# Kernel optimization log

Measured on AMD Instinct MI355X. Metric: run time of the kernel, lower is better.

Reference implementation:

```python
import jax, jax.numpy as jnp
import numpy as np

N = 50000        # nodes
E = 800000       # edges (avg degree 16)
NODE_D = 128     # node_attr_dim
EDGE_D = 16      # edge_attr_dim
HID = 300        # hidden_dim (module default)


def setup_inputs() -> dict:
    key = jax.random.key(0)
    ks = jax.random.split(key, 8)
    x = jax.random.normal(ks[0], (N, NODE_D), jnp.float32)
    edge_attr = jax.random.normal(ks[1], (E, EDGE_D), jnp.float32)
    edge_weight = jax.random.uniform(ks[2], (E,), jnp.float32)
    node_weight = jax.random.uniform(ks[3], (N,), jnp.float32)
    edge_index = jax.random.randint(ks[4], (2, E), 0, N, jnp.int32)
    # lin0: Linear(node_attr_dim + edge_attr_dim, hidden_dim)
    W0 = jax.random.normal(ks[5], (NODE_D + EDGE_D, HID), jnp.float32) / np.sqrt(NODE_D + EDGE_D)
    b0 = jnp.zeros((HID,), jnp.float32)
    # mp_layer.linear: Linear(hidden_dim, hidden_dim)
    W = jax.random.normal(ks[6], (HID, HID), jnp.float32) / np.sqrt(HID)
    b = jnp.zeros((HID,), jnp.float32)
    return dict(x=x, edge_attr=edge_attr, edge_weight=edge_weight,
                node_weight=node_weight, W0=W0, b0=b0, W=W, b=b,
                edge_index=edge_index)


def reference(x, edge_attr, edge_weight, node_weight, W0, b0, W, b, edge_index):
    src = edge_index[0]   # x_j (source, flow='source_to_target')
    dst = edge_index[1]   # aggregation target i
    n = x.shape[0]

    # --- isFirstLayer: weighted sum of incoming edge features, scattered at dst ---
    inc = jax.ops.segment_sum(edge_weight[:, None] * edge_attr, dst, num_segments=n)  # [N, EDGE_D]
    h0 = jax.nn.relu(jnp.concatenate([x, inc], axis=1) @ W0 + b0)                     # [N, HID]

    # --- MessagePassingLayer: message = edge_weight * x_j; aggr = mean at dst ---
    msg = edge_weight[:, None] * h0[src]                                              # [E, HID]
    agg = jax.ops.segment_sum(msg, dst, num_segments=n)                               # [N, HID]
    deg = jax.ops.segment_sum(jnp.ones((src.shape[0],), x.dtype), dst, num_segments=n)
    agg = agg / jnp.maximum(deg, 1.0)[:, None]  # scatter-mean (0 where no incoming edges)

    # --- update: relu(h0 + linear(aggr)) (add_residual=True) ---
    h = jax.nn.relu(h0 + agg @ W + b)
    # isLastLayer=False -> no node_weight scaling
    return (h, h0)
```

## Files before the change

kernel.cpp:

```cpp
#include <hip/hip_runtime.h>

#define NN 50000
#define NE 800000
#define ND 128
#define ED 16
#define HID 300
#define KP1 192
#define KP2 320
#define NP 320

#define SCAN_T 256
#define SCAN_B ((NN + SCAN_T - 1) / SCAN_T)

typedef __attribute__((ext_vector_type(8))) short short8;
typedef __attribute__((ext_vector_type(4))) float f32x4;

__device__ __forceinline__ unsigned short f2b(float f) {
    unsigned int u = __float_as_uint(f);
    u = (u + 0x7FFFu + ((u >> 16) & 1u)) >> 16;
    return (unsigned short)u;
}
__device__ __forceinline__ float blo(unsigned int u) {
    return __uint_as_float(u << 16);
}
__device__ __forceinline__ float bhi(unsigned int u) {
    return __uint_as_float(u & 0xffff0000u);
}

__device__ __forceinline__ void gload16(const void* g, void* l) {
    __builtin_amdgcn_global_load_lds(
        (const __attribute__((address_space(1))) void*)g,
        (__attribute__((address_space(3))) void*)l, 16, 0, 0);
}

__device__ __forceinline__ int block_iscan(int v, int tid) {
    int lane = tid & 63;
    #pragma unroll
    for (int off = 1; off < 64; off <<= 1) {
        int t = __shfl_up(v, off);
        if (lane >= off) v += t;
    }
    __shared__ int wsum[4];
    int wid = tid >> 6;
    if (lane == 63) wsum[wid] = v;
    __syncthreads();
    int add = 0;
    #pragma unroll
    for (int w = 0; w < 4; ++w)
        if (w < wid) add += wsum[w];
    return v + add;
}

__global__ void hist_kernel(const int* __restrict__ ei, int* __restrict__ rowptr) {
    int e = blockIdx.x * blockDim.x + threadIdx.x;
    if (e < NE) atomicAdd(&rowptr[ei[NE + e] + 1], 1);
}

__global__ __launch_bounds__(SCAN_T) void scan1(int* __restrict__ rowptr,
                                                int* __restrict__ blockSums) {
    int i = blockIdx.x * SCAN_T + threadIdx.x;
    int v = (i < NN) ? rowptr[1 + i] : 0;
    v = block_iscan(v, threadIdx.x);
    if (i < NN) rowptr[1 + i] = v;
    if (threadIdx.x == SCAN_T - 1) blockSums[blockIdx.x] = v;
}

__global__ __launch_bounds__(SCAN_T) void scan2(int* __restrict__ blockSums) {
    int t = threadIdx.x;
    int orig = (t < SCAN_B) ? blockSums[t] : 0;
    int v = block_iscan(orig, t);
    if (t < SCAN_B) blockSums[t] = v - orig;
}

__global__ __launch_bounds__(SCAN_T) void scan3(int* __restrict__ rowptr,
                                                const int* __restrict__ blockSums,
                                                int* __restrict__ cursor) {
    int i = blockIdx.x * SCAN_T + threadIdx.x;
    if (i < NN) {
        int v = rowptr[1 + i] + blockSums[blockIdx.x];
        rowptr[1 + i] = v;
        if (i + 1 < NN) cursor[i + 1] = v;
    }
    if (i == 0) cursor[0] = 0;
}

__global__ void fill_kernel(const int* __restrict__ ei, const float* __restrict__ ew,
                            int* __restrict__ cursor, uint4* __restrict__ csr) {
    int e = blockIdx.x * blockDim.x + threadIdx.x;
    if (e < NE) {
        int d = ei[NE + e];
        int pos = atomicAdd(&cursor[d], 1);
        uint4 q;
        q.x = (unsigned int)ei[e];
        q.y = (unsigned int)e;
        q.z = __float_as_uint(ew[e]);
        q.w = 0;
        csr[pos] = q;
    }
}

__global__ __launch_bounds__(256) void prep_kernel(
    const float* __restrict__ x,
    const float* __restrict__ edge_attr,
    const int* __restrict__ rowptr,
    const uint4* __restrict__ csr,
    unsigned short* __restrict__ A1) {
    int n = (blockIdx.x * blockDim.x + threadIdx.x) >> 6;
    int lane = threadIdx.x & 63;
    if (n >= NN) return;

    float2 v = *(const float2*)&x[(size_t)n * ND + lane * 2];
    unsigned int o = (unsigned int)f2b(v.x) | ((unsigned int)f2b(v.y) << 16);
    *(unsigned int*)&A1[(size_t)n * KP1 + lane * 2] = o;

    int g = lane >> 4, j = lane & 15;
    int lo = rowptr[n], hi = rowptr[n + 1];
    float s = 0.f;
    for (int k = lo + g; k < hi; k += 8) {
        int k1 = (k + 4 < hi) ? k + 4 : k;
        uint4 e0 = csr[k];
        uint4 e1 = csr[k1];
        float a0 = edge_attr[(size_t)e0.y * ED + j];
        float a1 = edge_attr[(size_t)e1.y * ED + j];
        s += __uint_as_float(e0.z) * a0;
        s += ((k + 4 < hi) ? __uint_as_float(e1.z) : 0.f) * a1;
    }
    s += __shfl_xor(s, 16);
    s += __shfl_xor(s, 32);
    if (lane < 16)
        A1[(size_t)n * KP1 + ND + lane] = f2b(s);
    else
        A1[(size_t)n * KP1 + ND + lane] = 0;
}

__global__ void castB0(const float* __restrict__ W0, unsigned short* __restrict__ B0T) {
    int n = blockIdx.x, k = threadIdx.x;
    float v = (n < HID && k < ND + ED) ? W0[(size_t)k * HID + n] : 0.f;
    B0T[(size_t)n * KP1 + k] = f2b(v);
}

__global__ void castB(const float* __restrict__ W, unsigned short* __restrict__ BT) {
    int n = blockIdx.x, k = threadIdx.x;
    float v = (n < HID && k < HID) ? W[(size_t)k * HID + n] : 0.f;
    BT[(size_t)n * KP2 + k] = f2b(v);
}

template <int MODE, int KP, int BN, int WM, int WN, int RPB>
__global__ __launch_bounds__(256) void gemm_stream(
    const unsigned short* __restrict__ A,
    const unsigned short* __restrict__ BT,
    const float* __restrict__ bias,
    const float* __restrict__ RES,
    float* __restrict__ C,
    unsigned short* __restrict__ h0b,
    int M)
{
    constexpr int CPR = KP / 8;
    constexpr int ACH = 32 * CPR;
    constexpr int BCH = BN * CPR;
    constexpr int AM  = 32 / (16 * WM);
    constexpr int BNW = BN / (16 * WN);
    __shared__ unsigned short Bs[BCH * 8];
    __shared__ unsigned short As[2][ACH * 8];

    const int tid = threadIdx.x;
    const int wave = tid >> 6, lane = tid & 63;
    const int wm = wave / WN, wn = wave % WN;
    const int quad = lane >> 4, lr = lane & 15;
    const int n00 = blockIdx.y * BN;
    const int rbase = blockIdx.x * RPB;
    const int rowend = min(rbase + RPB, M);
    const int nt = (rowend - rbase + 31) >> 5;

    #pragma unroll
    for (int rd = 0; rd < BCH / 256; ++rd) {
        int s = rd * 256 + tid;
        int row = s / CPR, c = s - row * CPR;
        int cs = (c & ~7) | ((c & 7) ^ (row & 7));
        gload16(&BT[(size_t)(n00 + row) * KP + cs * 8], &Bs[s * 8]);
    }
    auto stageA = [&](int buf, int mb) {
        #pragma unroll
        for (int rd = 0; rd < ACH / 256; ++rd) {
            int s = rd * 256 + tid;
            int row = s / CPR, c = s - row * CPR;
            int cs = (c & ~7) | ((c & 7) ^ (row & 7));
            int mg = mb + row; if (mg >= M) mg = M - 1;
            gload16(&A[(size_t)mg * KP + cs * 8], &As[buf][s * 8]);
        }
    };
    stageA(0, rbase);

    float bias_r[BNW];
    #pragma unroll
    for (int tn = 0; tn < BNW; ++tn) {
        int ng = n00 + wn * (BNW * 16) + tn * 16 + lr;
        bias_r[tn] = (ng < HID) ? bias[ng] : 0.f;
    }
    __syncthreads();

    int cur = 0;
    #pragma unroll 1
    for (int t = 0; t < nt; ++t) {
        const int mb = rbase + t * 32;
        if (t + 1 < nt) stageA(cur ^ 1, mb + 32);

        float res_r[AM][BNW][4];
        if (MODE == 1) {
            #pragma unroll
            for (int tm = 0; tm < AM; ++tm)
            #pragma unroll
            for (int tn = 0; tn < BNW; ++tn) {
                int ng = n00 + wn * (BNW * 16) + tn * 16 + lr;
                int ngc = ng < HID ? ng : HID - 1;
                #pragma unroll
                for (int r = 0; r < 4; ++r) {
                    int mg = mb + (wm * AM + tm) * 16 + quad * 4 + r;
                    int mgc = mg < M ? mg : M - 1;
                    res_r[tm][tn][r] = RES[(size_t)mgc * HID + ngc];
                }
            }
        }

        f32x4 acc[AM][BNW] = {};
        const int rm = lr & 7;
        #pragma unroll
        for (int tt = 0; tt < KP / 32; ++tt) {
            int cA = tt * 4 + quad;
            int sw8 = ((cA & ~7) | ((cA & 7) ^ rm)) * 8;
            short8 a[AM], b[BNW];
            #pragma unroll
            for (int tm = 0; tm < AM; ++tm) {
                int ar = (wm * AM + tm) * 16 + lr;
                a[tm] = *(const short8*)&As[cur][ar * KP + sw8];
            }
            #pragma unroll
            for (int tn = 0; tn < BNW; ++tn) {
                int br = wn * (BNW * 16) + tn * 16 + lr;
                b[tn] = *(const short8*)&Bs[br * KP + sw8];
            }
            #pragma unroll
            for (int tm = 0; tm < AM; ++tm)
                #pragma unroll
                for (int tn = 0; tn < BNW; ++tn)
                    acc[tm][tn] = __builtin_amdgcn_mfma_f32_16x16x32_bf16(
                        a[tm], b[tn], acc[tm][tn], 0, 0, 0);
        }

        #pragma unroll
        for (int tm = 0; tm < AM; ++tm)
        #pragma unroll
        for (int tn = 0; tn < BNW; ++tn) {
            int ng = n00 + wn * (BNW * 16) + tn * 16 + lr;
            #pragma unroll
            for (int r = 0; r < 4; ++r) {
                int mg = mb + (wm * AM + tm) * 16 + quad * 4 + r;
                if (mg < rowend && ng < HID) {
                    float v = acc[tm][tn][r] + bias_r[tn];
                    if (MODE == 1) v += res_r[tm][tn][r];
                    v = fmaxf(v, 0.f);
                    C[(size_t)mg * HID + ng] = v;
                    if (MODE == 0) h0b[(size_t)mg * NP + ng] = f2b(v);
                }
            }
        }
        __syncthreads();
        cur ^= 1;
    }
}

__device__ __forceinline__ void acc8(float* acc, float w, const uint4& r) {
    acc[0] += w * blo(r.x); acc[1] += w * bhi(r.x);
    acc[2] += w * blo(r.y); acc[3] += w * bhi(r.y);
    acc[4] += w * blo(r.z); acc[5] += w * bhi(r.z);
    acc[6] += w * blo(r.w); acc[7] += w * bhi(r.w);
}

__global__ __launch_bounds__(256) void agg_kernel(
    const unsigned short* __restrict__ h0b,
    const int* __restrict__ rowptr,
    const uint4* __restrict__ csr,
    unsigned short* __restrict__ aggB)
{
    int n = (blockIdx.x * blockDim.x + threadIdx.x) >> 6;
    int lane = threadIdx.x & 63;
    if (n >= NN) return;
    int lo = rowptr[n], hi = rowptr[n + 1];
    float acc[8] = {};
    const uint4* h4 = (const uint4*)h0b;
    bool act = lane < 40;
    for (int k = lo; k < hi; k += 4) {
        int k1 = (k + 1 < hi) ? k + 1 : k;
        int k2 = (k + 2 < hi) ? k + 2 : k;
        int k3 = (k + 3 < hi) ? k + 3 : k;
        uint4 p0 = csr[k], p1 = csr[k1], p2 = csr[k2], p3 = csr[k3];
        float w0 = __uint_as_float(p0.z);
        float w1 = (k + 1 < hi) ? __uint_as_float(p1.z) : 0.f;
        float w2 = (k + 2 < hi) ? __uint_as_float(p2.z) : 0.f;
        float w3 = (k + 3 < hi) ? __uint_as_float(p3.z) : 0.f;
        uint4 r0 = {0,0,0,0}, r1 = {0,0,0,0}, r2 = {0,0,0,0}, r3 = {0,0,0,0};
        if (act) {
            r0 = h4[(size_t)p0.x * 40 + lane];
            r1 = h4[(size_t)p1.x * 40 + lane];
            r2 = h4[(size_t)p2.x * 40 + lane];
            r3 = h4[(size_t)p3.x * 40 + lane];
        }
        acc8(acc, w0, r0);
        acc8(acc, w1, r1);
        acc8(acc, w2, r2);
        acc8(acc, w3, r3);
    }
    if (act) {
        float invd = 1.f / fmaxf((float)(hi - lo), 1.f);
        int cbase = lane * 8;
        unsigned int o[4];
        #pragma unroll
        for (int i = 0; i < 4; ++i) {
            int c0 = cbase + 2 * i, c1 = c0 + 1;
            unsigned int ulo = (c0 < HID) ? f2b(acc[2 * i] * invd) : 0;
            unsigned int uhi = (c1 < HID) ? f2b(acc[2 * i + 1] * invd) : 0;
            o[i] = ulo | (uhi << 16);
        }
        uint4* a4 = (uint4*)aggB;
        uint4 v; v.x = o[0]; v.y = o[1]; v.z = o[2]; v.w = o[3];
        a4[(size_t)n * 40 + lane] = v;
    }
}

extern "C" void kernel_launch(void* const* d_in, const int* in_sizes, int n_in,
                              void* d_out, int out_size, void* d_ws, size_t ws_size,
                              hipStream_t stream) {
    const float* x           = (const float*)d_in[0];
    const float* edge_attr   = (const float*)d_in[1];
    const float* edge_weight = (const float*)d_in[2];
    const float* W0 = (const float*)d_in[4];
    const float* b0 = (const float*)d_in[5];
    const float* W  = (const float*)d_in[6];
    const float* b  = (const float*)d_in[7];
    const int* ei   = (const int*)d_in[8];

    float* out = (float*)d_out;
    float* h  = out;
    float* h0 = out + (size_t)NN * HID;

    char* p = (char*)d_ws;
    auto alloc = [&](size_t bytes) { char* q = p; p += (bytes + 255) & ~(size_t)255; return q; };
    int*   rowptr  = (int*)  alloc((NN + 1) * sizeof(int));
    int*   cursor  = (int*)  alloc(NN * sizeof(int));
    int*   bsums   = (int*)  alloc(SCAN_B * sizeof(int));
    uint4* csr     = (uint4*)alloc((size_t)NE * sizeof(uint4));
    unsigned short* A1   = (unsigned short*)alloc((size_t)NN * KP1 * 2);
    unsigned short* h0b  = (unsigned short*)alloc((size_t)NN * NP * 2);
    unsigned short* aggB = (unsigned short*)alloc((size_t)NN * NP * 2);
    unsigned short* B0T  = (unsigned short*)alloc((size_t)NP * KP1 * 2);
    unsigned short* BT   = (unsigned short*)alloc((size_t)NP * KP2 * 2);

    hipMemsetAsync(rowptr, 0, (NN + 1) * sizeof(int), stream);
    hist_kernel<<<(NE + 255) / 256, 256, 0, stream>>>(ei, rowptr);
    scan1<<<SCAN_B, SCAN_T, 0, stream>>>(rowptr, bsums);
    scan2<<<1, SCAN_T, 0, stream>>>(bsums);
    scan3<<<SCAN_B, SCAN_T, 0, stream>>>(rowptr, bsums, cursor);
    fill_kernel<<<(NE + 255) / 256, 256, 0, stream>>>(ei, edge_weight, cursor, csr);
    castB0<<<NP, KP1, 0, stream>>>(W0, B0T);
    castB<<<NP, KP2, 0, stream>>>(W, BT);
    prep_kernel<<<(NN + 3) / 4, 256, 0, stream>>>(x, edge_attr, rowptr, csr, A1);

    gemm_stream<0, KP1, 320, 1, 4, 196><<<dim3(256, 1), 256, 0, stream>>>(
        A1, B0T, b0, nullptr, h0, h0b, NN);
    agg_kernel<<<(NN + 3) / 4, 256, 0, stream>>>(h0b, rowptr, csr, aggB);
    gemm_stream<1, KP2, 160, 2, 2, 391><<<dim3(128, 2), 256, 0, stream>>>(
        aggB, BT, b, h0, h, nullptr, NN);
}
```

Before: 447.2 us.

## Vectorize histogram, deepen gather unrolls, loop column tiles inside GEMM blocks

New measurement: 457.7 us. 2.4% more time.

```diff
diff --git a/kernel.cpp b/kernel.cpp
--- a/kernel.cpp
+++ b/kernel.cpp
@@ -52,8 +52,14 @@
 }
 
 __global__ void hist_kernel(const int* __restrict__ ei, int* __restrict__ rowptr) {
-    int e = blockIdx.x * blockDim.x + threadIdx.x;
-    if (e < NE) atomicAdd(&rowptr[ei[NE + e] + 1], 1);
+    int e4 = (blockIdx.x * blockDim.x + threadIdx.x) * 4;
+    if (e4 < NE) {
+        int4 d = *(const int4*)&ei[NE + e4];
+        atomicAdd(&rowptr[d.x + 1], 1);
+        atomicAdd(&rowptr[d.y + 1], 1);
+        atomicAdd(&rowptr[d.z + 1], 1);
+        atomicAdd(&rowptr[d.w + 1], 1);
+    }
 }
 
 __global__ __launch_bounds__(SCAN_T) void scan1(int* __restrict__ rowptr,
@@ -116,14 +122,20 @@
     int g = lane >> 4, j = lane & 15;
     int lo = rowptr[n], hi = rowptr[n + 1];
     float s = 0.f;
-    for (int k = lo + g; k < hi; k += 8) {
-        int k1 = (k + 4 < hi) ? k + 4 : k;
-        uint4 e0 = csr[k];
-        uint4 e1 = csr[k1];
+    for (int k = lo + g; k < hi; k += 16) {
+        int k1 = (k + 4  < hi) ? k + 4  : k;
+        int k2 = (k + 8  < hi) ? k + 8  : k;
+        int k3 = (k + 12 < hi) ? k + 12 : k;
+        uint4 e0 = csr[k],  e1 = csr[k1];
+        uint4 e2 = csr[k2], e3 = csr[k3];
         float a0 = edge_attr[(size_t)e0.y * ED + j];
         float a1 = edge_attr[(size_t)e1.y * ED + j];
+        float a2 = edge_attr[(size_t)e2.y * ED + j];
+        float a3 = edge_attr[(size_t)e3.y * ED + j];
         s += __uint_as_float(e0.z) * a0;
-        s += ((k + 4 < hi) ? __uint_as_float(e1.z) : 0.f) * a1;
+        s += ((k + 4  < hi) ? __uint_as_float(e1.z) : 0.f) * a1;
+        s += ((k + 8  < hi) ? __uint_as_float(e2.z) : 0.f) * a2;
+        s += ((k + 12 < hi) ? __uint_as_float(e3.z) : 0.f) * a3;
     }
     s += __shfl_xor(s, 16);
     s += __shfl_xor(s, 32);
@@ -145,7 +157,7 @@
     BT[(size_t)n * KP2 + k] = f2b(v);
 }
 
-template <int MODE, int KP, int BN, int WM, int WN, int RPB>
+template <int MODE, int KP, int BN, int WM, int WN, int RPB, int NY>
 __global__ __launch_bounds__(256) void gemm_stream(
     const unsigned short* __restrict__ A,
     const unsigned short* __restrict__ BT,
@@ -167,18 +179,10 @@
     const int wave = tid >> 6, lane = tid & 63;
     const int wm = wave / WN, wn = wave % WN;
     const int quad = lane >> 4, lr = lane & 15;
-    const int n00 = blockIdx.y * BN;
     const int rbase = blockIdx.x * RPB;
     const int rowend = min(rbase + RPB, M);
     const int nt = (rowend - rbase + 31) >> 5;
 
-    #pragma unroll
-    for (int rd = 0; rd < BCH / 256; ++rd) {
-        int s = rd * 256 + tid;
-        int row = s / CPR, c = s - row * CPR;
-        int cs = (c & ~7) | ((c & 7) ^ (row & 7));
-        gload16(&BT[(size_t)(n00 + row) * KP + cs * 8], &Bs[s * 8]);
-    }
     auto stageA = [&](int buf, int mb) {
         #pragma unroll
         for (int rd = 0; rd < ACH / 256; ++rd) {
@@ -189,83 +193,97 @@
             gload16(&A[(size_t)mg * KP + cs * 8], &As[buf][s * 8]);
         }
     };
-    stageA(0, rbase);
-
-    float bias_r[BNW];
-    #pragma unroll
-    for (int tn = 0; tn < BNW; ++tn) {
-        int ng = n00 + wn * (BNW * 16) + tn * 16 + lr;
-        bias_r[tn] = (ng < HID) ? bias[ng] : 0.f;
-    }
-    __syncthreads();
-
-    int cur = 0;
+
     #pragma unroll 1
-    for (int t = 0; t < nt; ++t) {
-        const int mb = rbase + t * 32;
-        if (t + 1 < nt) stageA(cur ^ 1, mb + 32);
-
-        float res_r[AM][BNW][4];
-        if (MODE == 1) {
+    for (int ny = 0; ny < NY; ++ny) {
+        const int n00 = ny * BN;
+        const int ncol = n00 + wn * (BNW * 16);
+
+        #pragma unroll
+        for (int rd = 0; rd < BCH / 256; ++rd) {
+            int s = rd * 256 + tid;
+            int row = s / CPR, c = s - row * CPR;
+            int cs = (c & ~7) | ((c & 7) ^ (row & 7));
+            gload16(&BT[(size_t)(n00 + row) * KP + cs * 8], &Bs[s * 8]);
+        }
+        stageA(0, rbase);
+
+        float bias_r[BNW];
+        #pragma unroll
+        for (int tn = 0; tn < BNW; ++tn) {
+            int ng = ncol + tn * 16 + lr;
+            bias_r[tn] = (ng < HID) ? bias[ng] : 0.f;
+        }
+        __syncthreads();
+
+        int cur = 0;
+        #pragma unroll 1
+        for (int t = 0; t < nt; ++t) {
+            const int mb = rbase + t * 32;
+            if (t + 1 < nt) stageA(cur ^ 1, mb + 32);
+
+            float res_r[AM][BNW][4];
+            if (MODE == 1) {
+                #pragma unroll
+                for (int tm = 0; tm < AM; ++tm)
+                #pragma unroll
+                for (int tn = 0; tn < BNW; ++tn) {
+                    int ng = ncol + tn * 16 + lr;
+                    int ngc = ng < HID ? ng : HID - 1;
+                    #pragma unroll
+                    for (int r = 0; r < 4; ++r) {
+                        int mg = mb + (wm * AM + tm) * 16 + quad * 4 + r;
+                        int mgc = mg < M ? mg : M - 1;
+                        res_r[tm][tn][r] = RES[(size_t)mgc * HID + ngc];
+                    }
+                }
+            }
+
+            f32x4 acc[AM][BNW] = {};
+            const int rm = lr & 7;
+            #pragma unroll
+            for (int tt = 0; tt < KP / 32; ++tt) {
+                int cA = tt * 4 + quad;
+                int sw8 = ((cA & ~7) | ((cA & 7) ^ rm)) * 8;
+                short8 a[AM], b[BNW];
+                #pragma unroll
+                for (int tm = 0; tm < AM; ++tm) {
+                    int ar = (wm * AM + tm) * 16 + lr;
+                    a[tm] = *(const short8*)&As[cur][ar * KP + sw8];
+                }
+                #pragma unroll
+                for (int tn = 0; tn < BNW; ++tn) {
+                    int br = wn * (BNW * 16) + tn * 16 + lr;
+                    b[tn] = *(const short8*)&Bs[br * KP + sw8];
+                }
+                #pragma unroll
+                for (int tm = 0; tm < AM; ++tm)
+                    #pragma unroll
+                    for (int tn = 0; tn < BNW; ++tn)
+                        acc[tm][tn] = __builtin_amdgcn_mfma_f32_16x16x32_bf16(
+                            a[tm], b[tn], acc[tm][tn], 0, 0, 0);
+            }
+
             #pragma unroll
             for (int tm = 0; tm < AM; ++tm)
             #pragma unroll
             for (int tn = 0; tn < BNW; ++tn) {
-                int ng = n00 + wn * (BNW * 16) + tn * 16 + lr;
-                int ngc = ng < HID ? ng : HID - 1;
+                int ng = ncol + tn * 16 + lr;
                 #pragma unroll
                 for (int r = 0; r < 4; ++r) {
                     int mg = mb + (wm * AM + tm) * 16 + quad * 4 + r;
-                    int mgc = mg < M ? mg : M - 1;
-                    res_r[tm][tn][r] = RES[(size_t)mgc * HID + ngc];
+                    if (mg < rowend && ng < HID) {
+                        float v = acc[tm][tn][r] + bias_r[tn];
+                        if (MODE == 1) v += res_r[tm][tn][r];
+                        v = fmaxf(v, 0.f);
+                        C[(size_t)mg * HID + ng] = v;
+                        if (MODE == 0) h0b[(size_t)mg * NP + ng] = f2b(v);
+                    }
                 }
             }
-        }
-
-        f32x4 acc[AM][BNW] = {};
-        const int rm = lr & 7;
-        #pragma unroll
-        for (int tt = 0; tt < KP / 32; ++tt) {
-            int cA = tt * 4 + quad;
-            int sw8 = ((cA & ~7) | ((cA & 7) ^ rm)) * 8;
-            short8 a[AM], b[BNW];
-            #pragma unroll
-            for (int tm = 0; tm < AM; ++tm) {
-                int ar = (wm * AM + tm) * 16 + lr;
-                a[tm] = *(const short8*)&As[cur][ar * KP + sw8];
-            }
-            #pragma unroll
-            for (int tn = 0; tn < BNW; ++tn) {
-                int br = wn * (BNW * 16) + tn * 16 + lr;
-                b[tn] = *(const short8*)&Bs[br * KP + sw8];
-            }
-            #pragma unroll
-            for (int tm = 0; tm < AM; ++tm)
-                #pragma unroll
-                for (int tn = 0; tn < BNW; ++tn)
-                    acc[tm][tn] = __builtin_amdgcn_mfma_f32_16x16x32_bf16(
-                        a[tm], b[tn], acc[tm][tn], 0, 0, 0);
-        }
-
-        #pragma unroll
-        for (int tm = 0; tm < AM; ++tm)
-        #pragma unroll
-        for (int tn = 0; tn < BNW; ++tn) {
-            int ng = n00 + wn * (BNW * 16) + tn * 16 + lr;
-            #pragma unroll
-            for (int r = 0; r < 4; ++r) {
-                int mg = mb + (wm * AM + tm) * 16 + quad * 4 + r;
-                if (mg < rowend && ng < HID) {
-                    float v = acc[tm][tn][r] + bias_r[tn];
-                    if (MODE == 1) v += res_r[tm][tn][r];
-                    v = fmaxf(v, 0.f);
-                    C[(size_t)mg * HID + ng] = v;
-                    if (MODE == 0) h0b[(size_t)mg * NP + ng] = f2b(v);
-                }
-            }
-        }
-        __syncthreads();
-        cur ^= 1;
+            __syncthreads();
+            cur ^= 1;
+        }
     }
 }
 
@@ -289,26 +307,39 @@
     float acc[8] = {};
     const uint4* h4 = (const uint4*)h0b;
     bool act = lane < 40;
-    for (int k = lo; k < hi; k += 4) {
-        int k1 = (k + 1 < hi) ? k + 1 : k;
-        int k2 = (k + 2 < hi) ? k + 2 : k;
-        int k3 = (k + 3 < hi) ? k + 3 : k;
-        uint4 p0 = csr[k], p1 = csr[k1], p2 = csr[k2], p3 = csr[k3];
+    for (int k = lo; k < hi; k += 8) {
+        uint4 p0 = csr[k];
+        uint4 p1 = csr[(k + 1 < hi) ? k + 1 : k];
+        uint4 p2 = csr[(k + 2 < hi) ? k + 2 : k];
+        uint4 p3 = csr[(k + 3 < hi) ? k + 3 : k];
+        uint4 p4 = csr[(k + 4 < hi) ? k + 4 : k];
+        uint4 p5 = csr[(k + 5 < hi) ? k + 5 : k];
+        uint4 p6 = csr[(k + 6 < hi) ? k + 6 : k];
+        uint4 p7 = csr[(k + 7 < hi) ? k + 7 : k];
         float w0 = __uint_as_float(p0.z);
         float w1 = (k + 1 < hi) ? __uint_as_float(p1.z) : 0.f;
         float w2 = (k + 2 < hi) ? __uint_as_float(p2.z) : 0.f;
         float w3 = (k + 3 < hi) ? __uint_as_float(p3.z) : 0.f;
+        float w4 = (k + 4 < hi) ? __uint_as_float(p4.z) : 0.f;
+        float w5 = (k + 5 < hi) ? __uint_as_float(p5.z) : 0.f;
+        float w6 = (k + 6 < hi) ? __uint_as_float(p6.z) : 0.f;
+        float w7 = (k + 7 < hi) ? __uint_as_float(p7.z) : 0.f;
         uint4 r0 = {0,0,0,0}, r1 = {0,0,0,0}, r2 = {0,0,0,0}, r3 = {0,0,0,0};
+        uint4 r4 = {0,0,0,0}, r5 = {0,0,0,0}, r6 = {0,0,0,0}, r7 = {0,0,0,0};
         if (act) {
             r0 = h4[(size_t)p0.x * 40 + lane];
             r1 = h4[(size_t)p1.x * 40 + lane];
             r2 = h4[(size_t)p2.x * 40 + lane];
             r3 = h4[(size_t)p3.x * 40 + lane];
-        }
-        acc8(acc, w0, r0);
-        acc8(acc, w1, r1);
-        acc8(acc, w2, r2);
-        acc8(acc, w3, r3);
+            r4 = h4[(size_t)p4.x * 40 + lane];
+            r5 = h4[(size_t)p5.x * 40 + lane];
+            r6 = h4[(size_t)p6.x * 40 + lane];
+            r7 = h4[(size_t)p7.x * 40 + lane];
+        }
+        acc8(acc, w0, r0); acc8(acc, w1, r1);
+        acc8(acc, w2, r2); acc8(acc, w3, r3);
+        acc8(acc, w4, r4); acc8(acc, w5, r5);
+        acc8(acc, w6, r6); acc8(acc, w7, r7);
     }
     if (act) {
         float invd = 1.f / fmaxf((float)(hi - lo), 1.f);
@@ -356,7 +387,7 @@
     unsigned short* BT   = (unsigned short*)alloc((size_t)NP * KP2 * 2);
 
     hipMemsetAsync(rowptr, 0, (NN + 1) * sizeof(int), stream);
-    hist_kernel<<<(NE + 255) / 256, 256, 0, stream>>>(ei, rowptr);
+    hist_kernel<<<(NE / 4 + 255) / 256, 256, 0, stream>>>(ei, rowptr);
     scan1<<<SCAN_B, SCAN_T, 0, stream>>>(rowptr, bsums);
     scan2<<<1, SCAN_T, 0, stream>>>(bsums);
     scan3<<<SCAN_B, SCAN_T, 0, stream>>>(rowptr, bsums, cursor);
@@ -365,9 +396,9 @@
     castB<<<NP, KP2, 0, stream>>>(W, BT);
     prep_kernel<<<(NN + 3) / 4, 256, 0, stream>>>(x, edge_attr, rowptr, csr, A1);
 
-    gemm_stream<0, KP1, 320, 1, 4, 196><<<dim3(256, 1), 256, 0, stream>>>(
+    gemm_stream<0, KP1, 320, 1, 4, 196, 1><<<dim3(256, 1), 256, 0, stream>>>(
         A1, B0T, b0, nullptr, h0, h0b, NN);
     agg_kernel<<<(NN + 3) / 4, 256, 0, stream>>>(h0b, rowptr, csr, aggB);
-    gemm_stream<1, KP2, 160, 2, 2, 391><<<dim3(128, 2), 256, 0, stream>>>(
+    gemm_stream<1, KP2, 160, 2, 2, 196, 2><<<dim3(256, 1), 256, 0, stream>>>(
         aggB, BT, b, h0, h, nullptr, NN);
 }
```
